# Kernel optimization log

Hardware: AMD Instinct MI355X
Metric: run time of the kernel (lower is better)

The kernel has to match this reference:

```python
import jax, jax.numpy as jnp
import numpy as np

N, E = 100000, 1600000
D_IN, H, C = 128, 4, 32
NEG_SLOPE = 0.2

def setup_inputs() -> dict:
    key = jax.random.key(0)
    ks = jax.random.split(key, 6)
    x = jax.random.normal(ks[0], (N, D_IN), dtype=jnp.float32)
    edge_index = jax.random.randint(ks[1], (2, E), 0, N, dtype=jnp.int64)
    s = 1.0 / np.sqrt(D_IN)
    W_l = jax.random.normal(ks[2], (D_IN, H * C), dtype=jnp.float32) * s
    W_r = jax.random.normal(ks[3], (D_IN, H * C), dtype=jnp.float32) * s
    att = jax.random.normal(ks[4], (H, C), dtype=jnp.float32) * (1.0 / np.sqrt(C))
    bias = jax.random.normal(ks[5], (H * C,), dtype=jnp.float32) * 0.01
    return {"x": x, "edge_index": edge_index, "W_l": W_l, "W_r": W_r, "att": att, "bias": bias}

def reference(x, edge_index, W_l, W_r, att, bias):
    # GATv2: e_ij = att . LeakyReLU(W_l x_j + W_r x_i); softmax over incoming edges of i;
    # out_i = sum_j alpha_ij * (W_l x_j); heads concatenated, then bias.
    src, dst = edge_index[0], edge_index[1]
    n = x.shape[0]
    xl = (x @ W_l).reshape(n, H, C)   # source transform (lin_l)
    xr = (x @ W_r).reshape(n, H, C)   # target transform (lin_r)
    xj = xl[src]                       # [E,H,C] gathered source feats
    xi = xr[dst]                       # [E,H,C] gathered target feats
    e = jax.nn.leaky_relu(xi + xj, NEG_SLOPE)
    score = jnp.einsum('ehc,hc->eh', e, att)          # [E,H]
    # segment softmax over destination nodes
    m = jax.ops.segment_max(score, dst, num_segments=n)  # [N,H]
    ex = jnp.exp(score - m[dst])
    denom = jax.ops.segment_sum(ex, dst, num_segments=n)  # [N,H]
    alpha = ex / (denom[dst] + 1e-16)                      # [E,H]
    out = jax.ops.segment_sum(alpha[..., None] * xj, dst, num_segments=n)  # [N,H,C]
    return out.reshape(n, H * C) + bias
```

## Files before the change

### kernel.cpp

```cpp
#include <hip/hip_runtime.h>
#include <hip/hip_bf16.h>
#include <math.h>

#define N_NODES 100000
#define E_EDGES 1600000
#define D 128
#define NEG_SLOPE 0.2f

#define BSH   5
#define BNODES 32
#define NBKT  3125
#define BCAP  832
#define SC_EPB 8192
#define SC_EPT 32
#define SC_BLOCKS ((E_EDGES + SC_EPB - 1) / SC_EPB)

typedef __bf16 bf16x8 __attribute__((ext_vector_type(8)));
typedef float f32x4 __attribute__((ext_vector_type(4)));
typedef float f32x2 __attribute__((ext_vector_type(2)));

__device__ __forceinline__ float bf2f(unsigned short u) {
    union { unsigned int i; float f; } x; x.i = ((unsigned int)u) << 16; return x.f;
}
__device__ __forceinline__ unsigned short f2bf(float f) {
    union { float f; unsigned int i; } x; x.f = f;
    unsigned int r = x.i + 0x7fffu + ((x.i >> 16) & 1u);
    return (unsigned short)(r >> 16);
}
__device__ __forceinline__ void unpack4p(uint2 u, f32x2* lo, f32x2* hi) {
    union { unsigned int i; float f; } a, b, c, d;
    a.i = u.x << 16; b.i = u.x & 0xffff0000u;
    c.i = u.y << 16; d.i = u.y & 0xffff0000u;
    *lo = (f32x2){a.f, b.f}; *hi = (f32x2){c.f, d.f};
}
__device__ __forceinline__ f32x2 pabs(f32x2 v) {
    union { f32x2 f; unsigned int u[2]; } x; x.f = v;
    x.u[0] &= 0x7fffffffu; x.u[1] &= 0x7fffffffu;
    return x.f;
}

__global__ void GATv2Conv_56908316672629_kernel(
    const unsigned int* ei_words, int* flags,
    const float* __restrict__ Wl, const float* __restrict__ Wr,
    unsigned short* __restrict__ wtg, int* __restrict__ bcur)
{
    __shared__ int cnt_edge;
    const int tid = threadIdx.x;
    const int bid = blockIdx.x;

    if (bid == 0) {
        for (int i = tid; i < NBKT; i += 256) bcur[i] = 0;
    }
    if (bid == 1) {
        if (tid == 0) cnt_edge = 0;
        __syncthreads();
        unsigned int w = ei_words[2 * tid + 1];
        if (w != 0u) atomicAdd(&cnt_edge, 1);
        __syncthreads();
        if (tid == 0) flags[0] = (cnt_edge == 0) ? 1 : 0;
    }

    const int gid = bid * 256 + tid;
    const int sel = gid >> 14;
    const int rem = gid & 16383;
    const int k = rem >> 7, n = rem & 127;
    const float* W = sel ? Wr : Wl;
    wtg[(size_t)sel * 16384 + n * 128 + k] = f2bf(W[k * 128 + n]);
}

__global__ __launch_bounds__(256) void gemm_f32_kernel(
    const float* __restrict__ X,
    const unsigned short* __restrict__ wtg,
    unsigned short* __restrict__ xl, unsigned short* __restrict__ xr,
    const unsigned int* __restrict__ ei, const int* __restrict__ flags,
    int* __restrict__ bcur, unsigned int* __restrict__ pairbuf)
{
    __shared__ union {
        struct {
            unsigned short Xs[128][136];
            unsigned short Cst[64][136];
        } g;
        struct { int h[NBKT]; int gbase[NBKT]; } sc;
    } sm;

    const int tid = threadIdx.x;

    if (blockIdx.x < SC_BLOCKS) {
        int* h = sm.sc.h;
        int* gbase = sm.sc.gbase;
        const int is64 = flags[0];
        const long long e0 = (long long)blockIdx.x * SC_EPB;

        unsigned int sv[SC_EPT], dv[SC_EPT];
#pragma unroll
        for (int j = 0; j < SC_EPT; ++j) {
            long long e = e0 + j * 256 + tid;
            unsigned int s = 0u, d = 0xffffffffu;
            if (e < E_EDGES) {
                if (is64) {
                    s = ((const uint2*)ei)[e].x;
                    d = ((const uint2*)ei)[E_EDGES + e].x;
                } else {
                    s = ei[e];
                    d = ei[E_EDGES + e];
                }
                if (s >= N_NODES || d >= N_NODES) d = 0xffffffffu;
            }
            sv[j] = s; dv[j] = d;
        }

        for (int i = tid; i < NBKT; i += 256) h[i] = 0;
        __syncthreads();

#pragma unroll
        for (int j = 0; j < SC_EPT; ++j)
            if (dv[j] != 0xffffffffu) atomicAdd(&h[dv[j] >> BSH], 1);
        __syncthreads();

        for (int i = tid; i < NBKT; i += 256) {
            int c = h[i];
            gbase[i] = c ? atomicAdd(&bcur[i], c) : 0;
            h[i] = 0;
        }
        __syncthreads();

#pragma unroll
        for (int j = 0; j < SC_EPT; ++j) {
            unsigned int d = dv[j];
            if (d != 0xffffffffu) {
                int b = (int)(d >> BSH);
                int r = gbase[b] + atomicAdd(&h[b], 1);
                if (r < BCAP)
                    pairbuf[(size_t)b * BCAP + r] = sv[j] | ((d & (BNODES - 1u)) << 24);
            }
        }
        return;
    }

    const int rowbase = (blockIdx.x - SC_BLOCKS) * 128;

    for (int c = tid; c < 4096; c += 256) {
        int r = c >> 5, k4 = (c & 31) << 2;
        int grow = rowbase + r;
        float4 v = make_float4(0.f, 0.f, 0.f, 0.f);
        if (grow < N_NODES) v = ((const float4*)(X + (size_t)grow * D))[c & 31];
        union { unsigned short us[4]; uint2 u2; } pk;
        pk.us[0] = f2bf(v.x); pk.us[1] = f2bf(v.y);
        pk.us[2] = f2bf(v.z); pk.us[3] = f2bf(v.w);
        *((uint2*)&sm.g.Xs[r][k4]) = pk.u2;
    }
    __syncthreads();

    const int wave = tid >> 6, lane = tid & 63;
    const int mrow = lane & 15, quad = lane >> 4;
    const int srow = tid >> 2, sseg = tid & 3;

    for (int sel = 0; sel < 2; ++sel) {
        const bf16x8* wt = (const bf16x8*)(wtg + (size_t)sel * 16384);
        unsigned short* out = sel ? xr : xl;

        f32x4 accA[8], accB[8];
#pragma unroll
        for (int i = 0; i < 8; ++i) {
            accA[i] = (f32x4){0.f, 0.f, 0.f, 0.f};
            accB[i] = (f32x4){0.f, 0.f, 0.f, 0.f};
        }

#pragma unroll
        for (int kk = 0; kk < 4; ++kk) {
            const int k0 = kk * 32 + quad * 8;
            bf16x8 afA = *(const bf16x8*)&sm.g.Xs[wave * 16 + mrow][k0];
            bf16x8 afB = *(const bf16x8*)&sm.g.Xs[64 + wave * 16 + mrow][k0];
            const bf16x8* wk = wt + mrow * 16 + kk * 4 + quad;
#pragma unroll
            for (int n0 = 0; n0 < 8; ++n0) {
                bf16x8 bfrag = wk[n0 * 256];
                accA[n0] = __builtin_amdgcn_mfma_f32_16x16x32_bf16(afA, bfrag, accA[n0], 0, 0, 0);
                accB[n0] = __builtin_amdgcn_mfma_f32_16x16x32_bf16(afB, bfrag, accB[n0], 0, 0, 0);
            }
        }

        __syncthreads();
        const int crow = wave * 16 + quad * 4;
#pragma unroll
        for (int n0 = 0; n0 < 8; ++n0) {
            int col = n0 * 16 + mrow;
#pragma unroll
            for (int r = 0; r < 4; ++r)
                sm.g.Cst[crow + r][col] = f2bf(accA[n0][r]);
        }
        __syncthreads();
        {
            int grow = rowbase + srow;
            if (grow < N_NODES) {
                uint4* dst = (uint4*)(out + (size_t)grow * D);
#pragma unroll
                for (int j = 0; j < 4; ++j)
                    dst[sseg * 4 + j] = *(const uint4*)&sm.g.Cst[srow][sseg * 32 + j * 8];
            }
        }

        __syncthreads();
#pragma unroll
        for (int n0 = 0; n0 < 8; ++n0) {
            int col = n0 * 16 + mrow;
#pragma unroll
            for (int r = 0; r < 4; ++r)
                sm.g.Cst[crow + r][col] = f2bf(accB[n0][r]);
        }
        __syncthreads();
        {
            int grow = rowbase + 64 + srow;
            if (grow < N_NODES) {
                uint4* dst = (uint4*)(out + (size_t)grow * D);
#pragma unroll
                for (int j = 0; j < 4; ++j)
                    dst[sseg * 4 + j] = *(const uint4*)&sm.g.Cst[srow][sseg * 32 + j * 8];
            }
        }
        __syncthreads();
    }
}

__global__ __launch_bounds__(256) void sort_agg_kernel(
    const int* __restrict__ bcur, const unsigned int* __restrict__ pairbuf,
    const unsigned short* __restrict__ xl, const unsigned short* __restrict__ xr,
    const float* __restrict__ att, const float* __restrict__ bias,
    float* __restrict__ out)
{
    __shared__ unsigned int stage[BCAP];
    __shared__ int sorted[BCAP];
    __shared__ int rs[BNODES], re[BNODES];
    __shared__ int cnt[BNODES];

    const int b = blockIdx.x;
    const int tid = threadIdx.x;
    int n = bcur[b]; if (n > BCAP) n = BCAP;
    const unsigned int* buf = pairbuf + (size_t)b * BCAP;

    for (int i = tid; i < n; i += 256) stage[i] = buf[i];
    if (tid < BNODES) cnt[tid] = 0;
    __syncthreads();

    for (int i = tid; i < n; i += 256) atomicAdd(&cnt[stage[i] >> 24], 1);
    __syncthreads();

    if (tid < BNODES) {
        int v = cnt[tid];
        int inc = v;
#pragma unroll
        for (int off = 1; off < BNODES; off <<= 1) {
            int u = __shfl_up(inc, off);
            if (tid >= off) inc += u;
        }
        rs[tid] = inc - v;
        re[tid] = inc;
        cnt[tid] = inc - v;
    }
    __syncthreads();

    for (int i = tid; i < n; i += 256) {
        unsigned int p = stage[i];
        int pos = atomicAdd(&cnt[p >> 24], 1);
        sorted[pos] = (int)(p & 0x00FFFFFFu);
    }
    __syncthreads();

    const int t = tid & 31;
    const int hw = tid >> 5;
    const int f0 = t * 4;

    const float4 av = *(const float4*)&att[f0];
    const f32x2 a60 = (f32x2){0.6f * av.x, 0.6f * av.y};
    const f32x2 a61 = (f32x2){0.6f * av.z, 0.6f * av.w};
    const f32x2 a40 = (f32x2){0.4f * av.x, 0.4f * av.y};
    const f32x2 a41 = (f32x2){0.4f * av.z, 0.4f * av.w};
    const uint2* xlp = (const uint2*)xl + (f0 >> 2);

#define ESCORE(u, xa0, xa1, pe)                                   \
    {                                                             \
        unpack4p(u, &xa0, &xa1);                                  \
        f32x2 v0 = xa0 + xr0, v1 = xa1 + xr1;                     \
        f32x2 pp = v0 * a60;                                      \
        pp += pabs(v0) * a40;                                     \
        pp += v1 * a61;                                           \
        pp += pabs(v1) * a41;                                     \
        pe = pp.x + pp.y;                                         \
    }

    for (int pass = 0; pass < 4; ++pass) {
        const int local = pass * 8 + hw;
        const int node = b * BNODES + local;

        f32x2 xr0, xr1;
        unpack4p(*(const uint2*)&xr[(size_t)node * D + f0], &xr0, &xr1);

        const int p0 = rs[local];
        const int p1 = re[local];

        float l = 0.f;
        f32x2 acc0 = (f32x2){0.f, 0.f}, acc1 = (f32x2){0.f, 0.f};

        int p = p0;
        for (; p + 4 <= p1; p += 4) {
            int s0 = sorted[p], s1 = sorted[p + 1], s2 = sorted[p + 2], s3 = sorted[p + 3];
            uint2 u0 = xlp[(size_t)s0 * 32];
            uint2 u1 = xlp[(size_t)s1 * 32];
            uint2 u2 = xlp[(size_t)s2 * 32];
            uint2 u3 = xlp[(size_t)s3 * 32];
            f32x2 xa0, xa1, xb0, xb1, xc0, xc1, xd0, xd1;
            float e0, e1, e2, e3;
            ESCORE(u0, xa0, xa1, e0);
            ESCORE(u1, xb0, xb1, e1);
            ESCORE(u2, xc0, xc1, e2);
            ESCORE(u3, xd0, xd1, e3);
#pragma unroll
            for (int off = 1; off < 8; off <<= 1) {
                e0 += __shfl_xor(e0, off);
                e1 += __shfl_xor(e1, off);
                e2 += __shfl_xor(e2, off);
                e3 += __shfl_xor(e3, off);
            }
            float w0 = __expf(e0), w1 = __expf(e1), w2 = __expf(e2), w3 = __expf(e3);
            l += (w0 + w1) + (w2 + w3);
            acc0 += w0 * xa0; acc1 += w0 * xa1;
            acc0 += w1 * xb0; acc1 += w1 * xb1;
            acc0 += w2 * xc0; acc1 += w2 * xc1;
            acc0 += w3 * xd0; acc1 += w3 * xd1;
        }
        for (; p < p1; ++p) {
            int s0 = sorted[p];
            uint2 u0 = xlp[(size_t)s0 * 32];
            f32x2 xa0, xa1;
            float e0;
            ESCORE(u0, xa0, xa1, e0);
#pragma unroll
            for (int off = 1; off < 8; off <<= 1) e0 += __shfl_xor(e0, off);
            float w0 = __expf(e0);
            l += w0;
            acc0 += w0 * xa0; acc1 += w0 * xa1;
        }

        const float inv = (l > 0.f) ? (1.f / l) : 0.f;
        const float4 bv = *(const float4*)&bias[f0];
        float4 o;
        o.x = fmaf(acc0.x, inv, bv.x);
        o.y = fmaf(acc0.y, inv, bv.y);
        o.z = fmaf(acc1.x, inv, bv.z);
        o.w = fmaf(acc1.y, inv, bv.w);
        *(float4*)&out[(size_t)node * D + f0] = o;
    }
#undef ESCORE
}

extern "C" void kernel_launch(void* const* d_in, const int* in_sizes, int n_in,
                              void* d_out, int out_size, void* d_ws, size_t ws_size,
                              hipStream_t stream)
{
    const float*        X    = (const float*)d_in[0];
    const unsigned int* ei   = (const unsigned int*)d_in[1];
    const float*        Wl   = (const float*)d_in[2];
    const float*        Wr   = (const float*)d_in[3];
    const float*        att  = (const float*)d_in[4];
    const float*        bias = (const float*)d_in[5];

    char* ws = (char*)d_ws;
    size_t off = 0;
    unsigned short* xl = (unsigned short*)(ws + off); off += (size_t)N_NODES * D * 2;
    unsigned short* xr = (unsigned short*)(ws + off); off += (size_t)N_NODES * D * 2;
    unsigned int* pairbuf = (unsigned int*)(ws + off); off += (size_t)NBKT * BCAP * 4;
    int* bcur     = (int*)(ws + off); off += (size_t)((NBKT + 255) & ~255) * 4;
    int* flags    = (int*)(ws + off); off += 256;
    unsigned short* wtg = (unsigned short*)(ws + off); off += 2 * 128 * 128 * 2;

    const int gb = (N_NODES + 127) / 128;

    GATv2Conv_56908316672629_kernel<<<128, 256, 0, stream>>>(ei, flags, Wl, Wr, wtg, bcur);

    gemm_f32_kernel<<<SC_BLOCKS + gb, 256, 0, stream>>>(
        X, wtg, xl, xr, ei, flags, bcur, pairbuf);

    sort_agg_kernel<<<NBKT, 256, 0, stream>>>(
        bcur, pairbuf, xl, xr, att, bias, (float*)d_out);
}
```

Measured before the change: 239.4 us.

## Scatter more edges per block with two-pass reread instead of register buffering

The edge-bucketing scatter blocks now each handle 65536 edges instead of 8192, looping over them twice. The first pass builds the shared-memory histogram and the second reloads the edge indices from global memory to place them. This cuts the number of scatter blocks and their global atomics on bucket cursors, and frees the 64 registers per thread that held edges. The cost is reading the edge indices twice and having only about 25 scatter blocks, which lowers parallelism while they run alongside the GEMM blocks.

```diff
diff --git a/kernel.cpp b/kernel.cpp
--- a/kernel.cpp
+++ b/kernel.cpp
@@ -11,8 +11,7 @@
 #define BNODES 32
 #define NBKT  3125
 #define BCAP  832
-#define SC_EPB 8192
-#define SC_EPT 32
+#define SC_EPB 65536
 #define SC_BLOCKS ((E_EDGES + SC_EPB - 1) / SC_EPB)
 
 typedef __bf16 bf16x8 __attribute__((ext_vector_type(8)));
@@ -90,31 +89,23 @@
         int* gbase = sm.sc.gbase;
         const int is64 = flags[0];
         const long long e0 = (long long)blockIdx.x * SC_EPB;
-
-        unsigned int sv[SC_EPT], dv[SC_EPT];
-#pragma unroll
-        for (int j = 0; j < SC_EPT; ++j) {
-            long long e = e0 + j * 256 + tid;
-            unsigned int s = 0u, d = 0xffffffffu;
-            if (e < E_EDGES) {
-                if (is64) {
-                    s = ((const uint2*)ei)[e].x;
-                    d = ((const uint2*)ei)[E_EDGES + e].x;
-                } else {
-                    s = ei[e];
-                    d = ei[E_EDGES + e];
-                }
-                if (s >= N_NODES || d >= N_NODES) d = 0xffffffffu;
-            }
-            sv[j] = s; dv[j] = d;
-        }
+        int n = E_EDGES - (int)e0; if (n > SC_EPB) n = SC_EPB;
 
         for (int i = tid; i < NBKT; i += 256) h[i] = 0;
         __syncthreads();
 
-#pragma unroll
-        for (int j = 0; j < SC_EPT; ++j)
-            if (dv[j] != 0xffffffffu) atomicAdd(&h[dv[j] >> BSH], 1);
+        for (int i = tid; i < n; i += 256) {
+            long long e = e0 + i;
+            unsigned int s, d;
+            if (is64) {
+                s = ((const uint2*)ei)[e].x;
+                d = ((const uint2*)ei)[E_EDGES + e].x;
+            } else {
+                s = ei[e];
+                d = ei[E_EDGES + e];
+            }
+            if (s < N_NODES && d < N_NODES) atomicAdd(&h[d >> BSH], 1);
+        }
         __syncthreads();
 
         for (int i = tid; i < NBKT; i += 256) {
@@ -124,14 +115,21 @@
         }
         __syncthreads();
 
-#pragma unroll
-        for (int j = 0; j < SC_EPT; ++j) {
-            unsigned int d = dv[j];
-            if (d != 0xffffffffu) {
+        for (int i = tid; i < n; i += 256) {
+            long long e = e0 + i;
+            unsigned int s, d;
+            if (is64) {
+                s = ((const uint2*)ei)[e].x;
+                d = ((const uint2*)ei)[E_EDGES + e].x;
+            } else {
+                s = ei[e];
+                d = ei[E_EDGES + e];
+            }
+            if (s < N_NODES && d < N_NODES) {
                 int b = (int)(d >> BSH);
                 int r = gbase[b] + atomicAdd(&h[b], 1);
                 if (r < BCAP)
-                    pairbuf[(size_t)b * BCAP + r] = sv[j] | ((d & (BNODES - 1u)) << 24);
+                    pairbuf[(size_t)b * BCAP + r] = s | ((d & (BNODES - 1u)) << 24);
             }
         }
         return;
```

After: 416.1 us. 73.8% more time.
